# Kernel tuning notes

Measured on AMD Instinct MI355X. Metric: run time of the kernel, lower is better.

## Reference

```python
import jax, jax.numpy as jnp
from jax import lax
import numpy as np

B, T, I, H, L, C = 64, 512, 128, 256, 2, 3


def _lstm_layer(x, W_ih, W_hh, b_ih, b_hh):
    # x: [B, T, in_dim]; W_ih: [4H, in_dim]; W_hh: [4H, H]
    # PyTorch gate order: i, f, g, o
    gates_x = jnp.einsum('bti,gi->btg', x, W_ih) + b_ih + b_hh  # [B, T, 4H]
    h0 = jnp.zeros((x.shape[0], W_hh.shape[1]), x.dtype)
    c0 = h0

    def step(carry, gx):
        h, c = carry
        g = gx + h @ W_hh.T  # [B, 4H]
        i, f, gg, o = jnp.split(g, 4, axis=-1)
        i = jax.nn.sigmoid(i)
        f = jax.nn.sigmoid(f)
        gg = jnp.tanh(gg)
        o = jax.nn.sigmoid(o)
        c = f * c + i * gg
        h = o * jnp.tanh(c)
        return (h, c), h

    _, hs = lax.scan(step, (h0, c0), jnp.swapaxes(gates_x, 0, 1))  # [T, B, H]
    return jnp.swapaxes(hs, 0, 1)  # [B, T, H]


def setup_inputs() -> dict:
    key = jax.random.key(0)
    ks = jax.random.split(key, 12)
    s = 1.0 / np.sqrt(H)
    u = lambda k, shape: jax.random.uniform(k, shape, jnp.float32, -s, s)
    return {
        'x': jax.random.normal(ks[0], (B, T, I), jnp.float32),
        'W_ih_0': u(ks[1], (4 * H, I)),
        'W_hh_0': u(ks[2], (4 * H, H)),
        'b_ih_0': u(ks[3], (4 * H,)),
        'b_hh_0': u(ks[4], (4 * H,)),
        'W_ih_1': u(ks[5], (4 * H, H)),
        'W_hh_1': u(ks[6], (4 * H, H)),
        'b_ih_1': u(ks[7], (4 * H,)),
        'b_hh_1': u(ks[8], (4 * H,)),
        'fc_w': u(ks[9], (C, H)),
        'fc_b': u(ks[10], (C,)),
    }


def reference(x, W_ih_0, W_hh_0, b_ih_0, b_hh_0, W_ih_1, W_hh_1, b_ih_1, b_hh_1, fc_w, fc_b):
    h = _lstm_layer(x, W_ih_0, W_hh_0, b_ih_0, b_hh_0)
    h = _lstm_layer(h, W_ih_1, W_hh_1, b_ih_1, b_hh_1)
    last = h[:, -1, :]                      # [B, H]
    logits = last @ fc_w.T + fc_b           # [B, C]
    return jax.nn.softmax(logits, axis=1)
```

## Files before the change

kernel.cpp:

```cpp
#include <hip/hip_runtime.h>
#include <cstdint>
#include <cstddef>

typedef _Float16 half2_t __attribute__((ext_vector_type(2)));
typedef _Float16 half8_t __attribute__((ext_vector_type(8)));
typedef float f32x4 __attribute__((ext_vector_type(4)));

static __device__ __forceinline__ float fdot2(half2_t a, half2_t b, float c) {
    return __builtin_amdgcn_fdot2(a, b, c, false);
}
static __device__ __forceinline__ half2_t h2(unsigned int u) {
    return __builtin_bit_cast(half2_t, u);
}
static __device__ __forceinline__ float sigm(float x) {
    return 1.f / (1.f + __expf(-x));
}
static __device__ __forceinline__ float tanh_fast(float x) {
    float ax = fabsf(x);
    float e = __expf(2.f * ax);
    float r = 1.f - 2.f / (e + 1.f);
    return copysignf(r, x);
}

__global__ __launch_bounds__(256) void prep_whh(const float* __restrict__ Whh,
                                                const float* __restrict__ bih,
                                                const float* __restrict__ bhh,
                                                uint4* __restrict__ Wp,
                                                float* __restrict__ bias) {
    int n = blockIdx.x * 256 + threadIdx.x;
    if (n < 1024) bias[n] = bih[n] + bhh[n];
    int p = n >> 9;
    int idx = n & 511;
    int qq = idx >> 8, jj = idx & 255;
    int g = p >> 4, u = p & 15;
    int row = g * 256 + jj;
    int kb = qq * 128 + u * 8;
    union { uint4 u4; _Float16 h[8]; } cv;
#pragma unroll
    for (int i = 0; i < 8; ++i) cv.h[i] = (_Float16)Whh[row * 256 + kb + i];
    Wp[p * 512 + idx] = cv.u4;
}

__global__ __launch_bounds__(256) void cvt_f16(const float* __restrict__ in,
                                               _Float16* __restrict__ out, int n4) {
    int i = blockIdx.x * 256 + threadIdx.x;
    if (i < n4) {
        float4 v = ((const float4*)in)[i];
        union { ushort4 u; _Float16 h[4]; } cv;
        cv.h[0] = (_Float16)v.x; cv.h[1] = (_Float16)v.y;
        cv.h[2] = (_Float16)v.z; cv.h[3] = (_Float16)v.w;
        ((ushort4*)out)[i] = cv.u;
    }
}

__global__ __launch_bounds__(256) void gemm_mfma(const _Float16* __restrict__ A,
                                                 const _Float16* __restrict__ Bw,
                                                 const float* __restrict__ bias,
                                                 float* __restrict__ Cmat, int K) {
    __shared__ _Float16 As[64][72];
    __shared__ _Float16 Bs[64][72];
    const int tid = threadIdx.x;
    const int wave = tid >> 6, lane = tid & 63;
    const int quad = lane >> 4, l16 = lane & 15;
    const int m0 = blockIdx.x * 64, n0 = blockIdx.y * 64;
    const int sr = tid >> 2;
    const int sc = (tid & 3) * 16;

    f32x4 acc[4] = {};

    for (int k0 = 0; k0 < K; k0 += 64) {
        const uint4 a0v = *(const uint4*)(A + (size_t)(m0 + sr) * K + k0 + sc);
        const uint4 a1v = *(const uint4*)(A + (size_t)(m0 + sr) * K + k0 + sc + 8);
        const uint4 b0v = *(const uint4*)(Bw + (size_t)(n0 + sr) * K + k0 + sc);
        const uint4 b1v = *(const uint4*)(Bw + (size_t)(n0 + sr) * K + k0 + sc + 8);
        __syncthreads();
        *(uint4*)&As[sr][sc] = a0v;
        *(uint4*)&As[sr][sc + 8] = a1v;
        *(uint4*)&Bs[sr][sc] = b0v;
        *(uint4*)&Bs[sr][sc + 8] = b1v;
        __syncthreads();
#pragma unroll
        for (int kc = 0; kc < 64; kc += 32) {
            half8_t af = *(const half8_t*)&As[wave * 16 + l16][kc + quad * 8];
#pragma unroll
            for (int nb = 0; nb < 4; ++nb) {
                half8_t bf = *(const half8_t*)&Bs[nb * 16 + l16][kc + quad * 8];
                acc[nb] = __builtin_amdgcn_mfma_f32_16x16x32_f16(af, bf, acc[nb], 0, 0, 0);
            }
        }
    }
#pragma unroll
    for (int nb = 0; nb < 4; ++nb) {
#pragma unroll
        for (int i = 0; i < 4; ++i) {
            int row = m0 + wave * 16 + quad * 4 + i;
            int col = n0 + nb * 16 + l16;
            Cmat[(size_t)row * 1024 + col] = acc[nb][i] + bias[col];
        }
    }
}

__global__ __launch_bounds__(512, 2)
void lstm_scan(const float* __restrict__ gx,
               const uint4* __restrict__ Wp,
               _Float16* __restrict__ h_out,
               int store_all) {
    const int b = blockIdx.x;
    const int tid = threadIdx.x;
    const int q = tid >> 8;
    const int j = tid & 255;

    __shared__ uint4 wlds[16 * 512];
    __shared__ f32x4 pex[512] __attribute__((aligned(16)));
    __shared__ _Float16 hbuf[2][256] __attribute__((aligned(16)));
    __shared__ _Float16 hist[8][256] __attribute__((aligned(16)));

#pragma unroll
    for (int p = 0; p < 16; ++p) wlds[p * 512 + tid] = Wp[(48 + p) * 512 + tid];
    uint4 wreg[48];
#pragma unroll
    for (int p = 0; p < 48; ++p) wreg[p] = Wp[p * 512 + tid];

    if (tid < 256) hbuf[0][tid] = (_Float16)0.f;
    float c = 0.f;
    const float* gxb = gx + (size_t)b * 512 * 1024 + (size_t)(q * 512 + j);
    float gA = gxb[0], gB = gxb[256];
    __syncthreads();

    for (int t = 0; t < 512; ++t) {
        float gA_n = 0.f, gB_n = 0.f;
        if (t < 511) {
            gA_n = gxb[(size_t)(t + 1) * 1024];
            gB_n = gxb[(size_t)(t + 1) * 1024 + 256];
        }

        const char* hp = (const char*)&hbuf[t & 1][0] + q * 256;
        float a0 = 0.f, a1 = 0.f, a2 = 0.f, a3 = 0.f;
#pragma unroll
        for (int u = 0; u < 16; ++u) {
            const uint4 hv = *(const uint4*)(hp + u * 16);
            const uint4 w0 = wreg[u];
            const uint4 w1 = wreg[16 + u];
            const uint4 w2 = wreg[32 + u];
            const uint4 w3 = wlds[u * 512 + tid];
            a0 = fdot2(h2(w0.x), h2(hv.x), a0);
            a1 = fdot2(h2(w1.x), h2(hv.x), a1);
            a2 = fdot2(h2(w2.x), h2(hv.x), a2);
            a3 = fdot2(h2(w3.x), h2(hv.x), a3);
            a0 = fdot2(h2(w0.y), h2(hv.y), a0);
            a1 = fdot2(h2(w1.y), h2(hv.y), a1);
            a2 = fdot2(h2(w2.y), h2(hv.y), a2);
            a3 = fdot2(h2(w3.y), h2(hv.y), a3);
            a0 = fdot2(h2(w0.z), h2(hv.z), a0);
            a1 = fdot2(h2(w1.z), h2(hv.z), a1);
            a2 = fdot2(h2(w2.z), h2(hv.z), a2);
            a3 = fdot2(h2(w3.z), h2(hv.z), a3);
            a0 = fdot2(h2(w0.w), h2(hv.w), a0);
            a1 = fdot2(h2(w1.w), h2(hv.w), a1);
            a2 = fdot2(h2(w2.w), h2(hv.w), a2);
            a3 = fdot2(h2(w3.w), h2(hv.w), a3);
        }
        if (q == 0) { a0 += gA; a1 += gB; }
        else        { a2 += gA; a3 += gB; }

        f32x4 pv = {a0, a1, a2, a3};
        pex[tid] = pv;
        gA = gA_n; gB = gB_n;
        __syncthreads();

        if (tid < 256) {
            const f32x4 v0 = pex[tid];
            const f32x4 v1 = pex[256 + tid];
            const float ai = v0[0] + v1[0];
            const float af = v0[1] + v1[1];
            const float ag = v0[2] + v1[2];
            const float ao = v0[3] + v1[3];
            const float iv = sigm(ai);
            const float fv = sigm(af);
            const float gv = tanh_fast(ag);
            const float ov = sigm(ao);
            c = fv * c + iv * gv;
            const _Float16 hh = (_Float16)(ov * tanh_fast(c));
            hbuf[(t + 1) & 1][tid] = hh;
            if (store_all) hist[t & 7][tid] = hh;
        }
        __syncthreads();

        if (store_all && (t & 7) == 7) {
            const uint2 v = ((const uint2*)hist)[tid];
            *(uint2*)(h_out + (size_t)b * 512 * 256 + (size_t)(t - 7) * 256 + tid * 4) = v;
        }
    }
    if (!store_all && tid < 256) {
        h_out[(size_t)b * 256 + tid] = hbuf[0][tid];
    }
}

__global__ __launch_bounds__(64) void fc_softmax(const _Float16* __restrict__ hlast,
                                                 const float* __restrict__ fcw,
                                                 const float* __restrict__ fcb,
                                                 float* __restrict__ out) {
    const int b = blockIdx.x;
    const int lane = threadIdx.x;
    const _Float16* h = hlast + (size_t)b * 256;
    float p0 = 0.f, p1 = 0.f, p2 = 0.f;
    for (int k = lane; k < 256; k += 64) {
        float hv = (float)h[k];
        p0 += hv * fcw[k];
        p1 += hv * fcw[256 + k];
        p2 += hv * fcw[512 + k];
    }
#pragma unroll
    for (int off = 32; off > 0; off >>= 1) {
        p0 += __shfl_down(p0, off);
        p1 += __shfl_down(p1, off);
        p2 += __shfl_down(p2, off);
    }
    if (lane == 0) {
        float l0 = p0 + fcb[0], l1 = p1 + fcb[1], l2 = p2 + fcb[2];
        float m = fmaxf(l0, fmaxf(l1, l2));
        float e0 = __expf(l0 - m), e1 = __expf(l1 - m), e2 = __expf(l2 - m);
        float s = 1.f / (e0 + e1 + e2);
        out[b * 3 + 0] = e0 * s;
        out[b * 3 + 1] = e1 * s;
        out[b * 3 + 2] = e2 * s;
    }
}

extern "C" void kernel_launch(void* const* d_in, const int* in_sizes, int n_in,
                              void* d_out, int out_size, void* d_ws, size_t ws_size,
                              hipStream_t stream) {
    const float* x    = (const float*)d_in[0];
    const float* Wih0 = (const float*)d_in[1];
    const float* Whh0 = (const float*)d_in[2];
    const float* bih0 = (const float*)d_in[3];
    const float* bhh0 = (const float*)d_in[4];
    const float* Wih1 = (const float*)d_in[5];
    const float* Whh1 = (const float*)d_in[6];
    const float* bih1 = (const float*)d_in[7];
    const float* bhh1 = (const float*)d_in[8];
    const float* fcw  = (const float*)d_in[9];
    const float* fcb  = (const float*)d_in[10];
    float* out = (float*)d_out;

    char* ws = (char*)d_ws;
    float* gx        = (float*)ws;     ws += (size_t)32768 * 1024 * 4;
    _Float16* h0f    = (_Float16*)ws;  ws += (size_t)32768 * 256 * 2;
    _Float16* xh     = (_Float16*)ws;  ws += (size_t)32768 * 128 * 2;
    _Float16* hlast  = (_Float16*)ws;  ws += (size_t)64 * 256 * 2;
    _Float16* Wih0h  = (_Float16*)ws;  ws += (size_t)1024 * 128 * 2;
    _Float16* Wih1h  = (_Float16*)ws;  ws += (size_t)1024 * 256 * 2;
    uint4* Wp0       = (uint4*)ws;     ws += (size_t)1024 * 256 * 2;
    uint4* Wp1       = (uint4*)ws;     ws += (size_t)1024 * 256 * 2;
    float* bias0     = (float*)ws;     ws += 4096;
    float* bias1     = (float*)ws;     ws += 4096;

    prep_whh<<<128, 256, 0, stream>>>(Whh0, bih0, bhh0, Wp0, bias0);
    prep_whh<<<128, 256, 0, stream>>>(Whh1, bih1, bhh1, Wp1, bias1);
    cvt_f16<<<4096, 256, 0, stream>>>(x, xh, 32768 * 128 / 4);
    cvt_f16<<<128, 256, 0, stream>>>(Wih0, Wih0h, 1024 * 128 / 4);
    cvt_f16<<<256, 256, 0, stream>>>(Wih1, Wih1h, 1024 * 256 / 4);

    gemm_mfma<<<dim3(512, 16), 256, 0, stream>>>(xh, Wih0h, bias0, gx, 128);
    lstm_scan<<<64, 512, 0, stream>>>(gx, Wp0, h0f, 1);

    gemm_mfma<<<dim3(512, 16), 256, 0, stream>>>(h0f, Wih1h, bias1, gx, 256);
    lstm_scan<<<64, 512, 0, stream>>>(gx, Wp1, hlast, 0);

    fc_softmax<<<64, 64, 0, stream>>>(hlast, fcw, fcb, out);
}
```

Baseline: 1.693 ms.

## Reduce LSTM gate partial sums via wave shuffles, one barrier per step

Remaps threads so the two K-halves of each hidden unit sit in the same wavefront 32 lanes apart, and combines the partial dot products with xor-shuffles instead of an LDS exchange. Every lane now computes the gate nonlinearities redundantly, which removes the pex buffer and one of the two block barriers per timestep. The h-history buffer is doubled to 16 slots so the flush of 8 finished rows does not race with writes to the next rows, and the weight packing is reordered to match the new lane layout. It adds duplicated activation math and a hand-written waitcnt+barrier in place of __syncthreads.

```diff
diff --git a/kernel.cpp b/kernel.cpp
--- a/kernel.cpp
+++ b/kernel.cpp
@@ -30,15 +30,16 @@
     int n = blockIdx.x * 256 + threadIdx.x;
     if (n < 1024) bias[n] = bih[n] + bhh[n];
     int p = n >> 9;
-    int idx = n & 511;
-    int qq = idx >> 8, jj = idx & 255;
+    int tid = n & 511;
     int g = p >> 4, u = p & 15;
-    int row = g * 256 + jj;
-    int kb = qq * 128 + u * 8;
+    int w = tid >> 6, l = tid & 63;
+    int q = l >> 5, l31 = l & 31;
+    int row = g * 256 + w * 32 + l31;
+    int kb = q * 128 + u * 8;
     union { uint4 u4; _Float16 h[8]; } cv;
 #pragma unroll
     for (int i = 0; i < 8; ++i) cv.h[i] = (_Float16)Whh[row * 256 + kb + i];
-    Wp[p * 512 + idx] = cv.u4;
+    Wp[p * 512 + tid] = cv.u4;
 }
 
 __global__ __launch_bounds__(256) void cvt_f16(const float* __restrict__ in,
@@ -107,13 +108,15 @@
                int store_all) {
     const int b = blockIdx.x;
     const int tid = threadIdx.x;
-    const int q = tid >> 8;
-    const int j = tid & 255;
+    const int w = tid >> 6;
+    const int l = tid & 63;
+    const int q = l >> 5;
+    const int l31 = l & 31;
+    const int j = w * 32 + l31;
 
     __shared__ uint4 wlds[16 * 512];
-    __shared__ f32x4 pex[512] __attribute__((aligned(16)));
     __shared__ _Float16 hbuf[2][256] __attribute__((aligned(16)));
-    __shared__ _Float16 hist[8][256] __attribute__((aligned(16)));
+    __shared__ _Float16 hist[16][256] __attribute__((aligned(16)));
 
 #pragma unroll
     for (int p = 0; p < 16; ++p) wlds[p * 512 + tid] = Wp[(48 + p) * 512 + tid];
@@ -162,33 +165,32 @@
         }
         if (q == 0) { a0 += gA; a1 += gB; }
         else        { a2 += gA; a3 += gB; }
-
-        f32x4 pv = {a0, a1, a2, a3};
-        pex[tid] = pv;
+        a0 += __shfl_xor(a0, 32);
+        a1 += __shfl_xor(a1, 32);
+        a2 += __shfl_xor(a2, 32);
+        a3 += __shfl_xor(a3, 32);
+
+        const float iv = sigm(a0);
+        const float fv = sigm(a1);
+        const float gv = tanh_fast(a2);
+        const float ov = sigm(a3);
+        c = fv * c + iv * gv;
+        const _Float16 hh = (_Float16)(ov * tanh_fast(c));
+
+        if (q == 0) hbuf[(t + 1) & 1][j] = hh;
+        else if (store_all) hist[t & 15][j] = hh;
         gA = gA_n; gB = gB_n;
-        __syncthreads();
-
-        if (tid < 256) {
-            const f32x4 v0 = pex[tid];
-            const f32x4 v1 = pex[256 + tid];
-            const float ai = v0[0] + v1[0];
-            const float af = v0[1] + v1[1];
-            const float ag = v0[2] + v1[2];
-            const float ao = v0[3] + v1[3];
-            const float iv = sigm(ai);
-            const float fv = sigm(af);
-            const float gv = tanh_fast(ag);
-            const float ov = sigm(ao);
-            c = fv * c + iv * gv;
-            const _Float16 hh = (_Float16)(ov * tanh_fast(c));
-            hbuf[(t + 1) & 1][tid] = hh;
-            if (store_all) hist[t & 7][tid] = hh;
-        }
-        __syncthreads();
+
+        asm volatile("s_waitcnt lgkmcnt(0)" ::: "memory");
+        __builtin_amdgcn_s_barrier();
+        asm volatile("" ::: "memory");
 
         if (store_all && (t & 7) == 7) {
-            const uint2 v = ((const uint2*)hist)[tid];
-            *(uint2*)(h_out + (size_t)b * 512 * 256 + (size_t)(t - 7) * 256 + tid * 4) = v;
+            const int s = tid >> 6, e = tid & 63;
+            const int s0 = (t - 7) & 15;
+            const uint2 v = *(const uint2*)&hist[s0 + s][e * 4];
+            *(uint2*)(h_out + (size_t)b * 512 * 256 +
+                      (size_t)(t - 7 + s) * 256 + e * 4) = v;
         }
     }
     if (!store_all && tid < 256) {
```

After: 1.793 ms. +5.9%, slower.
